# Kernel tuning notes

Measured on AMD Instinct MI355X. Metric: run time of the kernel, lower is better.

## Reference

```python
import jax, jax.numpy as jnp
import numpy as np

N = 100000
E = 1600000
F_IN = 128
DIM = 32
C = 2
BN_EPS = 1e-5


def setup_inputs() -> dict:
    key = jax.random.key(0)
    ks = jax.random.split(key, 24)
    s = 0.1
    inp = {
        'x': jax.random.normal(ks[0], (N, F_IN), dtype=jnp.float32),
        'edge_index': jax.random.randint(ks[1], (2, E), 0, N, dtype=jnp.int64),
        'edge_attr': jax.random.normal(ks[2], (E, 1), dtype=jnp.float32),
        'batch': jnp.zeros((N,), dtype=jnp.int64),
        # GIN layer 1 MLP: Linear(F_IN, DIM) -> ReLU -> Linear(DIM, DIM)
        'w1a': jax.random.normal(ks[3], (F_IN, DIM), dtype=jnp.float32) * s,
        'b1a': jnp.zeros((DIM,), dtype=jnp.float32),
        'w1b': jax.random.normal(ks[4], (DIM, DIM), dtype=jnp.float32) * s,
        'b1b': jnp.zeros((DIM,), dtype=jnp.float32),
        'g1': jnp.ones((DIM,), dtype=jnp.float32),
        'be1': jnp.zeros((DIM,), dtype=jnp.float32),
        # GIN layer 2
        'w2a': jax.random.normal(ks[5], (DIM, DIM), dtype=jnp.float32) * s,
        'b2a': jnp.zeros((DIM,), dtype=jnp.float32),
        'w2b': jax.random.normal(ks[6], (DIM, DIM), dtype=jnp.float32) * s,
        'b2b': jnp.zeros((DIM,), dtype=jnp.float32),
        'g2': jnp.ones((DIM,), dtype=jnp.float32),
        'be2': jnp.zeros((DIM,), dtype=jnp.float32),
        # GIN layer 3
        'w3a': jax.random.normal(ks[7], (DIM, DIM), dtype=jnp.float32) * s,
        'b3a': jnp.zeros((DIM,), dtype=jnp.float32),
        'w3b': jax.random.normal(ks[8], (DIM, DIM), dtype=jnp.float32) * s,
        'b3b': jnp.zeros((DIM,), dtype=jnp.float32),
        'g3': jnp.ones((DIM,), dtype=jnp.float32),
        'be3': jnp.zeros((DIM,), dtype=jnp.float32),
        # head
        'fw1': jax.random.normal(ks[9], (DIM, DIM), dtype=jnp.float32) * s,
        'fb1': jnp.zeros((DIM,), dtype=jnp.float32),
        'fw2': jax.random.normal(ks[10], (DIM, C), dtype=jnp.float32) * s,
        'fb2': jnp.zeros((C,), dtype=jnp.float32),
    }
    return inp


def _gin(x, src, dst, wa, ba, wb, bb):
    # GINConv with eps=0: h_i = MLP((1+eps)*x_i + sum_{j->i} x_j)
    agg = jax.ops.segment_sum(x[src], dst, num_segments=N)
    h = x + agg
    h = jax.nn.relu(h @ wa + ba) @ wb + bb
    return h


def _bn(h, g, b):
    # BatchNorm1d with batch statistics (training-mode normalization)
    mu = h.mean(axis=0)
    var = h.var(axis=0)  # biased, matches torch normalization
    return (h - mu) * jax.lax.rsqrt(var + BN_EPS) * g + b


def reference(x, edge_index, edge_attr, batch,
              w1a, b1a, w1b, b1b, g1, be1,
              w2a, b2a, w2b, b2b, g2, be2,
              w3a, b3a, w3b, b3b, g3, be3,
              fw1, fb1, fw2, fb2):
    src, dst = edge_index[0], edge_index[1]
    h = _bn(jax.nn.relu(_gin(x, src, dst, w1a, b1a, w1b, b1b)), g1, be1)
    h = _bn(jax.nn.relu(_gin(h, src, dst, w2a, b2a, w2b, b2b)), g2, be2)
    h = _bn(jax.nn.relu(_gin(h, src, dst, w3a, b3a, w3b, b3b)), g3, be3)
    h = jax.nn.relu(h @ fw1 + fb1)
    # dropout treated as identity (eval mode / deterministic reference)
    return h @ fw2 + fb2
```

## Files before the change

kernel.cpp:

```cpp
#include <hip/hip_runtime.h>

#define NNODES 100000
#define NEDGES 1600000
#define FIN 128
#define DIM 32
#define BN_EPS 1e-5f
#define NBUK ((NNODES + 255) >> 8)
#define CH 8192

__device__ __forceinline__ unsigned int f2bf2(float a, float b) {
    union { float f; unsigned int u; } ua, ub;
    ua.f = a; ub.f = b;
    const unsigned int ra = (ua.u + 0x7FFFu + ((ua.u >> 16) & 1u)) >> 16;
    const unsigned int rb = (ub.u + 0x7FFFu + ((ub.u >> 16) & 1u)) >> 16;
    return ra | (rb << 16);
}
__device__ __forceinline__ float bf_lo(unsigned int u) {
    union { unsigned int u; float f; } c; c.u = u << 16; return c.f;
}
__device__ __forceinline__ float bf_hi(unsigned int u) {
    union { unsigned int u; float f; } c; c.u = u & 0xFFFF0000u; return c.f;
}

__global__ void __launch_bounds__(256) k_proj1(const float* __restrict__ x,
                                               const float* __restrict__ w,
                                               unsigned int* __restrict__ zb) {
    const int i = blockIdx.x * 256 + threadIdx.x;
    if (i >= NNODES) return;
    const float4* xp = reinterpret_cast<const float4*>(x + (size_t)i * FIN);
    float acc[DIM];
#pragma unroll
    for (int c = 0; c < DIM; ++c) acc[c] = 0.f;

    for (int k0 = 0; k0 < FIN; k0 += 32) {
        float4 r[8];
#pragma unroll
        for (int q = 0; q < 8; ++q) r[q] = xp[k0 / 4 + q];
        float a[32];
#pragma unroll
        for (int q = 0; q < 8; ++q) {
            a[q * 4 + 0] = r[q].x; a[q * 4 + 1] = r[q].y;
            a[q * 4 + 2] = r[q].z; a[q * 4 + 3] = r[q].w;
        }
#pragma unroll
        for (int kk = 0; kk < 32; ++kk) {
            const float tk = a[kk];
#pragma unroll
            for (int c = 0; c < DIM; ++c)
                acc[c] += tk * w[(k0 + kk) * DIM + c];
        }
    }
    uint4* zp = reinterpret_cast<uint4*>(zb + (size_t)i * 16);
#pragma unroll
    for (int q = 0; q < 4; ++q)
        zp[q] = make_uint4(f2bf2(acc[q * 8 + 0], acc[q * 8 + 1]),
                           f2bf2(acc[q * 8 + 2], acc[q * 8 + 3]),
                           f2bf2(acc[q * 8 + 4], acc[q * 8 + 5]),
                           f2bf2(acc[q * 8 + 6], acc[q * 8 + 7]));
}

__global__ void k_bhist(const int* __restrict__ ei, int* __restrict__ bucketCnt) {
    __shared__ int cnt[NBUK];
    for (int i = threadIdx.x; i < NBUK; i += 256) cnt[i] = 0;
    __syncthreads();
    const int tid    = blockIdx.x * blockDim.x + threadIdx.x;
    const int stride = gridDim.x * blockDim.x;
    for (int e = tid; e < NEDGES; e += stride)
        atomicAdd(&cnt[ei[NEDGES + e] >> 8], 1);
    __syncthreads();
    for (int i = threadIdx.x; i < NBUK; i += 256)
        if (cnt[i]) atomicAdd(&bucketCnt[i], cnt[i]);
}

__global__ void k_bscan(const int* __restrict__ bucketCnt,
                        int* __restrict__ bbase, int* __restrict__ gcur,
                        float* __restrict__ stats) {
    __shared__ int sbuf[512];
    const int t = threadIdx.x;
    if (t < 192) stats[t] = 0.f;
    const int v = (t < NBUK) ? bucketCnt[t] : 0;
    sbuf[t] = v;
    __syncthreads();
    for (int off = 1; off < 512; off <<= 1) {
        const int u = (t >= off) ? sbuf[t - off] : 0;
        __syncthreads();
        sbuf[t] += u;
        __syncthreads();
    }
    if (t < NBUK) { const int ex = sbuf[t] - v; bbase[t] = ex; gcur[t] = ex; }
    if (t == 0) bbase[NBUK] = NEDGES;
}

__global__ void __launch_bounds__(256) k_bscatter(const int* __restrict__ ei,
                                                  int* __restrict__ gcur,
                                                  int* __restrict__ bucketed) {
    __shared__ int cnt[NBUK];
    __shared__ int base[NBUK];
    const int start = blockIdx.x * CH;
    const int end   = min(start + CH, NEDGES);
    for (int i = threadIdx.x; i < NBUK; i += 256) cnt[i] = 0;
    __syncthreads();
    for (int e = start + threadIdx.x; e < end; e += 256)
        atomicAdd(&cnt[ei[NEDGES + e] >> 8], 1);
    __syncthreads();
    for (int i = threadIdx.x; i < NBUK; i += 256) {
        const int c = cnt[i];
        base[i] = c ? atomicAdd(&gcur[i], c) : 0;
        cnt[i] = 0;
    }
    __syncthreads();
    for (int e = start + threadIdx.x; e < end; e += 256) {
        const int s = ei[e];
        const int d = ei[NEDGES + e];
        const int b = d >> 8;
        const int p = atomicAdd(&cnt[b], 1);
        bucketed[base[b] + p] = s | ((d & 255) << 17);
    }
}

__global__ void __launch_bounds__(256) k_bfill(const int* __restrict__ bucketed,
                                               const int* __restrict__ bbase,
                                               int* __restrict__ rowstart,
                                               int* __restrict__ deg,
                                               int* __restrict__ sorted_src) {
    __shared__ int dcnt[256], dsc[256], cur[256];
    const int b  = blockIdx.x;
    const int lo = bbase[b];
    const int hi = bbase[b + 1];
    const int t  = threadIdx.x;
    dcnt[t] = 0;
    __syncthreads();
    for (int p = lo + t; p < hi; p += 256)
        atomicAdd(&dcnt[bucketed[p] >> 17], 1);
    __syncthreads();
    const int myc = dcnt[t];
    dsc[t] = myc;
    __syncthreads();
    for (int off = 1; off < 256; off <<= 1) {
        const int u = (t >= off) ? dsc[t - off] : 0;
        __syncthreads();
        dsc[t] += u;
        __syncthreads();
    }
    const int ex = dsc[t] - myc;
    const int node = (b << 8) + t;
    if (node < NNODES) { rowstart[node] = lo + ex; deg[node] = myc; }
    dcnt[t] = ex;
    cur[t] = 0;
    __syncthreads();
    for (int p = lo + t; p < hi; p += 256) {
        const int v = bucketed[p];
        const int dl = v >> 17;
        const int pos = atomicAdd(&cur[dl], 1);
        sorted_src[lo + dcnt[dl] + pos] = v & 0x1FFFF;
    }
}

__global__ void k_gather_t(const unsigned int* __restrict__ zb,
                           const int* __restrict__ rowstart,
                           const int* __restrict__ deg,
                           const int* __restrict__ sorted_src,
                           const float* __restrict__ ba,
                           float* __restrict__ tbuf) {
    const int lane = threadIdx.x & 31;
    const int g    = lane >> 2;
    const int q    = lane & 3;
    const float4 baA = reinterpret_cast<const float4*>(ba)[q * 2];
    const float4 baB = reinterpret_cast<const float4*>(ba)[q * 2 + 1];
    const uint4* z4 = reinterpret_cast<const uint4*>(zb);
    const int hw  = (blockIdx.x * blockDim.x + threadIdx.x) >> 5;
    const int nhw = (gridDim.x * blockDim.x) >> 5;

    for (int i = hw; i < NNODES; i += nhw) {
        const int base = rowstart[i];
        const int cnt  = deg[i];
        float4 aA = make_float4(0.f, 0.f, 0.f, 0.f);
        float4 aB = make_float4(0.f, 0.f, 0.f, 0.f);
        float4 bA = make_float4(0.f, 0.f, 0.f, 0.f);
        float4 bB = make_float4(0.f, 0.f, 0.f, 0.f);
        for (int k0 = 0; k0 < cnt; k0 += 32) {
            int e = 0;
            if (k0 + lane < cnt) e = sorted_src[base + k0 + lane];
            const int m = min(32, cnt - k0);
            for (int j = 0; j < m; j += 16) {
                const int s0 = __shfl(e, j + g, 32);
                const int s1 = __shfl(e, j + 8 + g, 32);
                if (j + g < m) {
                    const uint4 v = z4[s0 * 4 + q];
                    aA.x += bf_lo(v.x); aA.y += bf_hi(v.x);
                    aA.z += bf_lo(v.y); aA.w += bf_hi(v.y);
                    aB.x += bf_lo(v.z); aB.y += bf_hi(v.z);
                    aB.z += bf_lo(v.w); aB.w += bf_hi(v.w);
                }
                if (j + 8 + g < m) {
                    const uint4 v = z4[s1 * 4 + q];
                    bA.x += bf_lo(v.x); bA.y += bf_hi(v.x);
                    bA.z += bf_lo(v.y); bA.w += bf_hi(v.y);
                    bB.x += bf_lo(v.z); bB.y += bf_hi(v.z);
                    bB.z += bf_lo(v.w); bB.w += bf_hi(v.w);
                }
            }
        }
        aA.x += bA.x; aA.y += bA.y; aA.z += bA.z; aA.w += bA.w;
        aB.x += bB.x; aB.y += bB.y; aB.z += bB.z; aB.w += bB.w;
#pragma unroll
        for (int mask = 4; mask <= 16; mask <<= 1) {
            aA.x += __shfl_xor(aA.x, mask, 32);
            aA.y += __shfl_xor(aA.y, mask, 32);
            aA.z += __shfl_xor(aA.z, mask, 32);
            aA.w += __shfl_xor(aA.w, mask, 32);
            aB.x += __shfl_xor(aB.x, mask, 32);
            aB.y += __shfl_xor(aB.y, mask, 32);
            aB.z += __shfl_xor(aB.z, mask, 32);
            aB.w += __shfl_xor(aB.w, mask, 32);
        }
        if (g == 0) {
            const uint4 v = z4[i * 4 + q];
            float4 tA, tB;
            tA.x = fmaxf(bf_lo(v.x) + aA.x + baA.x, 0.f);
            tA.y = fmaxf(bf_hi(v.x) + aA.y + baA.y, 0.f);
            tA.z = fmaxf(bf_lo(v.y) + aA.z + baA.z, 0.f);
            tA.w = fmaxf(bf_hi(v.y) + aA.w + baA.w, 0.f);
            tB.x = fmaxf(bf_lo(v.z) + aB.x + baB.x, 0.f);
            tB.y = fmaxf(bf_hi(v.z) + aB.y + baB.y, 0.f);
            tB.z = fmaxf(bf_lo(v.w) + aB.z + baB.z, 0.f);
            tB.w = fmaxf(bf_hi(v.w) + aB.w + baB.w, 0.f);
            float4* tp = reinterpret_cast<float4*>(tbuf + (size_t)i * DIM);
            tp[q * 2 + 0] = tA;
            tp[q * 2 + 1] = tB;
        }
    }
}

__global__ void __launch_bounds__(256) k_mlp2(float* __restrict__ hbuf,
                                              const float* __restrict__ wb,
                                              const float* __restrict__ bb,
                                              float* __restrict__ stats) {
    __shared__ float ssum[DIM], ssq[DIM];
    if (threadIdx.x < DIM) { ssum[threadIdx.x] = 0.f; ssq[threadIdx.x] = 0.f; }
    __syncthreads();

    const int i = blockIdx.x * 256 + threadIdx.x;
    const bool valid = i < NNODES;

    float a[DIM];
    if (valid) {
        const float4* tp = reinterpret_cast<const float4*>(hbuf + (size_t)i * DIM);
        float4 r[8];
#pragma unroll
        for (int qq = 0; qq < 8; ++qq) r[qq] = tp[qq];
#pragma unroll
        for (int qq = 0; qq < 8; ++qq) {
            a[qq * 4 + 0] = r[qq].x; a[qq * 4 + 1] = r[qq].y;
            a[qq * 4 + 2] = r[qq].z; a[qq * 4 + 3] = r[qq].w;
        }
    } else {
#pragma unroll
        for (int k = 0; k < DIM; ++k) a[k] = 0.f;
    }

    float acc[DIM];
#pragma unroll
    for (int c = 0; c < DIM; ++c) acc[c] = bb[c];
#pragma unroll
    for (int k = 0; k < DIM; ++k) {
        const float tk = a[k];
#pragma unroll
        for (int c = 0; c < DIM; ++c)
            acc[c] += tk * wb[k * DIM + c];
    }
#pragma unroll
    for (int c = 0; c < DIM; ++c) acc[c] = valid ? fmaxf(acc[c], 0.f) : 0.f;

    if (valid) {
        float4* hp = reinterpret_cast<float4*>(hbuf + (size_t)i * DIM);
#pragma unroll
        for (int qq = 0; qq < 8; ++qq)
            hp[qq] = make_float4(acc[qq * 4], acc[qq * 4 + 1], acc[qq * 4 + 2], acc[qq * 4 + 3]);
    }

    const int lane = threadIdx.x & 63;
    float lsum = 0.f, lsq = 0.f;
#pragma unroll
    for (int c = 0; c < DIM; ++c) {
        float v  = acc[c];
        float w2 = acc[c] * acc[c];
#pragma unroll
        for (int off = 1; off < 64; off <<= 1) {
            v  += __shfl_xor(v, off);
            w2 += __shfl_xor(w2, off);
        }
        if (lane == c) { lsum = v; lsq = w2; }
    }
    if (lane < DIM) {
        atomicAdd(&ssum[lane], lsum);
        atomicAdd(&ssq[lane], lsq);
    }
    __syncthreads();
    if (threadIdx.x < DIM) {
        atomicAdd(&stats[threadIdx.x],       ssum[threadIdx.x]);
        atomicAdd(&stats[DIM + threadIdx.x], ssq[threadIdx.x]);
    }
}

__global__ void __launch_bounds__(256) k_projbn(const float* __restrict__ h,
                                                const float* __restrict__ stats,
                                                const float* __restrict__ g,
                                                const float* __restrict__ be,
                                                const float* __restrict__ wa,
                                                unsigned int* __restrict__ zb) {
    const int t  = threadIdx.x;
    const int i  = blockIdx.x * 128 + (t & 127);
    const int ch = (t >> 7) * 16;
    if (i >= NNODES) return;
    const float4* hp = reinterpret_cast<const float4*>(h + (size_t)i * DIM);
    float4 r[8];
#pragma unroll
    for (int q = 0; q < 8; ++q) r[q] = hp[q];
    float a[DIM];
#pragma unroll
    for (int q = 0; q < 8; ++q) {
        a[q * 4 + 0] = r[q].x; a[q * 4 + 1] = r[q].y;
        a[q * 4 + 2] = r[q].z; a[q * 4 + 3] = r[q].w;
    }
    float acc[16];
#pragma unroll
    for (int c = 0; c < 16; ++c) acc[c] = 0.f;
#pragma unroll
    for (int k = 0; k < DIM; ++k) {
        const float mu  = stats[k] * (1.f / NNODES);
        const float var = stats[DIM + k] * (1.f / NNODES) - mu * mu;
        const float ss  = g[k] * rsqrtf(var + BN_EPS);
        const float st  = be[k] - mu * ss;
        const float tk  = a[k] * ss + st;
        const float* wr = wa + k * DIM + ch;
#pragma unroll
        for (int c = 0; c < 16; ++c)
            acc[c] += tk * wr[c];
    }
    uint4* zp = reinterpret_cast<uint4*>(zb + (size_t)i * 16 + ch / 2);
    zp[0] = make_uint4(f2bf2(acc[0], acc[1]),  f2bf2(acc[2], acc[3]),
                       f2bf2(acc[4], acc[5]),  f2bf2(acc[6], acc[7]));
    zp[1] = make_uint4(f2bf2(acc[8], acc[9]),  f2bf2(acc[10], acc[11]),
                       f2bf2(acc[12], acc[13]), f2bf2(acc[14], acc[15]));
}

__global__ void __launch_bounds__(256) k_head(const float* __restrict__ h,
                                              const float* __restrict__ stats,
                                              const float* __restrict__ g,
                                              const float* __restrict__ be,
                                              const float* __restrict__ fw1,
                                              const float* __restrict__ fb1,
                                              const float* __restrict__ fw2,
                                              const float* __restrict__ fb2,
                                              float* __restrict__ out) {
    const int i = blockIdx.x * 256 + threadIdx.x;
    if (i >= NNODES) return;
    const float4* hp = reinterpret_cast<const float4*>(h + (size_t)i * DIM);
    float4 r[8];
#pragma unroll
    for (int q = 0; q < 8; ++q) r[q] = hp[q];
    float a[DIM];
#pragma unroll
    for (int q = 0; q < 8; ++q) {
        a[q * 4 + 0] = r[q].x; a[q * 4 + 1] = r[q].y;
        a[q * 4 + 2] = r[q].z; a[q * 4 + 3] = r[q].w;
    }
    float acc[DIM];
#pragma unroll
    for (int c = 0; c < DIM; ++c) acc[c] = fb1[c];
#pragma unroll
    for (int k = 0; k < DIM; ++k) {
        const float mu  = stats[k] * (1.f / NNODES);
        const float var = stats[DIM + k] * (1.f / NNODES) - mu * mu;
        const float ss  = g[k] * rsqrtf(var + BN_EPS);
        const float st  = be[k] - mu * ss;
        const float tk  = a[k] * ss + st;
#pragma unroll
        for (int c = 0; c < DIM; ++c)
            acc[c] += tk * fw1[k * DIM + c];
    }
    float o0 = fb2[0], o1 = fb2[1];
#pragma unroll
    for (int c = 0; c < DIM; ++c) {
        const float u = fmaxf(acc[c], 0.f);
        o0 += u * fw2[c * 2 + 0];
        o1 += u * fw2[c * 2 + 1];
    }
    *reinterpret_cast<float2*>(&out[i * 2]) = make_float2(o0, o1);
}

extern "C" void kernel_launch(void* const* d_in, const int* in_sizes, int n_in,
                              void* d_out, int out_size, void* d_ws, size_t ws_size,
                              hipStream_t stream) {
    const float* x   = (const float*)d_in[0];
    const int*   ei  = (const int*)d_in[1];
    const float* w1a = (const float*)d_in[4];
    const float* b1a = (const float*)d_in[5];
    const float* w1b = (const float*)d_in[6];
    const float* b1b = (const float*)d_in[7];
    const float* g1  = (const float*)d_in[8];
    const float* be1 = (const float*)d_in[9];
    const float* w2a = (const float*)d_in[10];
    const float* b2a = (const float*)d_in[11];
    const float* w2b = (const float*)d_in[12];
    const float* b2b = (const float*)d_in[13];
    const float* g2  = (const float*)d_in[14];
    const float* be2 = (const float*)d_in[15];
    const float* w3a = (const float*)d_in[16];
    const float* b3a = (const float*)d_in[17];
    const float* w3b = (const float*)d_in[18];
    const float* b3b = (const float*)d_in[19];
    const float* g3  = (const float*)d_in[20];
    const float* be3 = (const float*)d_in[21];
    const float* fw1 = (const float*)d_in[22];
    const float* fb1 = (const float*)d_in[23];
    const float* fw2 = (const float*)d_in[24];
    const float* fb2 = (const float*)d_in[25];
    float* out = (float*)d_out;

    float* ws = (float*)d_ws;
    const size_t nf = (size_t)NNODES * DIM;
    unsigned int* zb = (unsigned int*)ws;
    float* h     = ws + nf;
    int*   bucketed = (int*)h;
    float* stats = ws + 2 * nf;
    int* rowstart   = (int*)(ws + 2 * nf + 192);
    int* deg        = rowstart + NNODES;
    int* sorted_src = deg + NNODES;
    int* bucketCnt  = sorted_src + NEDGES;
    int* bbase      = bucketCnt + NBUK;
    int* gcur       = bbase + NBUK + 1;

    const int TB = 256, NB_G = 2048;
    const int NB_TPN = (NNODES + 255) / 256;
    const int NB_PB  = (NNODES + 127) / 128;

    hipMemsetAsync(bucketCnt, 0, NBUK * sizeof(int), stream);

    k_bhist<<<512, TB, 0, stream>>>(ei, bucketCnt);
    k_bscan<<<1, 512, 0, stream>>>(bucketCnt, bbase, gcur, stats);
    k_bscatter<<<(NEDGES + CH - 1) / CH, TB, 0, stream>>>(ei, gcur, bucketed);
    k_bfill<<<NBUK, TB, 0, stream>>>(bucketed, bbase, rowstart, deg, sorted_src);

    k_proj1<<<NB_TPN, TB, 0, stream>>>(x, w1a, zb);
    k_gather_t<<<NB_G, TB, 0, stream>>>(zb, rowstart, deg, sorted_src, b1a, h);
    k_mlp2<<<NB_TPN, TB, 0, stream>>>(h, w1b, b1b, stats + 0);
    k_projbn<<<NB_PB, TB, 0, stream>>>(h, stats + 0, g1, be1, w2a, zb);
    k_gather_t<<<NB_G, TB, 0, stream>>>(zb, rowstart, deg, sorted_src, b2a, h);
    k_mlp2<<<NB_TPN, TB, 0, stream>>>(h, w2b, b2b, stats + 64);
    k_projbn<<<NB_PB, TB, 0, stream>>>(h, stats + 64, g2, be2, w3a, zb);
    k_gather_t<<<NB_G, TB, 0, stream>>>(zb, rowstart, deg, sorted_src, b3a, h);
    k_mlp2<<<NB_TPN, TB, 0, stream>>>(h, w3b, b3b, stats + 128);
    k_head<<<NB_TPN, TB, 0, stream>>>(h, stats + 128, g3, be3,
                                      fw1, fb1, fw2, fb2, out);
}
```

Before: 329.6 us.

## Split proj1 K-dimension across 4 lanes and simplify gather index loading

k_proj1 now assigns four lanes per node, each covering a quarter of the 128-wide input, with float4 weight loads and a shuffle reduction at the end. This gives four times the threads and makes the x reads from neighbouring lanes contiguous instead of strided per node. The gather kernel drops the 32-wide index preload plus shuffle broadcast and has each lane load its source index directly in 16-edge steps. This removes shuffle and branching overhead but issues more small redundant index loads.

Result: slower. 491.3 us (+49.1%).

```diff
diff --git a/kernel.cpp b/kernel.cpp
--- a/kernel.cpp
+++ b/kernel.cpp
@@ -25,38 +25,55 @@
 __global__ void __launch_bounds__(256) k_proj1(const float* __restrict__ x,
                                                const float* __restrict__ w,
                                                unsigned int* __restrict__ zb) {
-    const int i = blockIdx.x * 256 + threadIdx.x;
-    if (i >= NNODES) return;
-    const float4* xp = reinterpret_cast<const float4*>(x + (size_t)i * FIN);
+    const int t    = threadIdx.x;
+    const int l    = t & 63;
+    const int node = blockIdx.x * 64 + (t >> 6) * 16 + (l >> 2);
+    const int kq   = l & 3;
+    const bool valid = node < NNODES;
+
     float acc[DIM];
 #pragma unroll
     for (int c = 0; c < DIM; ++c) acc[c] = 0.f;
 
-    for (int k0 = 0; k0 < FIN; k0 += 32) {
+    if (valid) {
+        const float4* xp = reinterpret_cast<const float4*>(x + (size_t)node * FIN + kq * 32);
         float4 r[8];
 #pragma unroll
-        for (int q = 0; q < 8; ++q) r[q] = xp[k0 / 4 + q];
+        for (int q = 0; q < 8; ++q) r[q] = xp[q];
         float a[32];
 #pragma unroll
         for (int q = 0; q < 8; ++q) {
             a[q * 4 + 0] = r[q].x; a[q * 4 + 1] = r[q].y;
             a[q * 4 + 2] = r[q].z; a[q * 4 + 3] = r[q].w;
         }
+        const float4* w4 = reinterpret_cast<const float4*>(w) + (size_t)kq * 32 * 8;
 #pragma unroll
         for (int kk = 0; kk < 32; ++kk) {
             const float tk = a[kk];
 #pragma unroll
-            for (int c = 0; c < DIM; ++c)
-                acc[c] += tk * w[(k0 + kk) * DIM + c];
-        }
-    }
-    uint4* zp = reinterpret_cast<uint4*>(zb + (size_t)i * 16);
-#pragma unroll
-    for (int q = 0; q < 4; ++q)
-        zp[q] = make_uint4(f2bf2(acc[q * 8 + 0], acc[q * 8 + 1]),
-                           f2bf2(acc[q * 8 + 2], acc[q * 8 + 3]),
-                           f2bf2(acc[q * 8 + 4], acc[q * 8 + 5]),
-                           f2bf2(acc[q * 8 + 6], acc[q * 8 + 7]));
+            for (int cq = 0; cq < 8; ++cq) {
+                const float4 wv = w4[kk * 8 + cq];
+                acc[cq * 4 + 0] += tk * wv.x;
+                acc[cq * 4 + 1] += tk * wv.y;
+                acc[cq * 4 + 2] += tk * wv.z;
+                acc[cq * 4 + 3] += tk * wv.w;
+            }
+        }
+    }
+#pragma unroll
+    for (int c = 0; c < DIM; ++c) {
+        acc[c] += __shfl_xor(acc[c], 1);
+        acc[c] += __shfl_xor(acc[c], 2);
+    }
+    if (valid && kq == 0) {
+        uint4* zp = reinterpret_cast<uint4*>(zb + (size_t)node * 16);
+#pragma unroll
+        for (int q = 0; q < 4; ++q)
+            zp[q] = make_uint4(f2bf2(acc[q * 8 + 0], acc[q * 8 + 1]),
+                               f2bf2(acc[q * 8 + 2], acc[q * 8 + 3]),
+                               f2bf2(acc[q * 8 + 4], acc[q * 8 + 5]),
+                               f2bf2(acc[q * 8 + 6], acc[q * 8 + 7]));
+    }
 }
 
 __global__ void k_bhist(const int* __restrict__ ei, int* __restrict__ bucketCnt) {
@@ -178,27 +195,24 @@
         float4 aB = make_float4(0.f, 0.f, 0.f, 0.f);
         float4 bA = make_float4(0.f, 0.f, 0.f, 0.f);
         float4 bB = make_float4(0.f, 0.f, 0.f, 0.f);
-        for (int k0 = 0; k0 < cnt; k0 += 32) {
-            int e = 0;
-            if (k0 + lane < cnt) e = sorted_src[base + k0 + lane];
-            const int m = min(32, cnt - k0);
-            for (int j = 0; j < m; j += 16) {
-                const int s0 = __shfl(e, j + g, 32);
-                const int s1 = __shfl(e, j + 8 + g, 32);
-                if (j + g < m) {
-                    const uint4 v = z4[s0 * 4 + q];
-                    aA.x += bf_lo(v.x); aA.y += bf_hi(v.x);
-                    aA.z += bf_lo(v.y); aA.w += bf_hi(v.y);
-                    aB.x += bf_lo(v.z); aB.y += bf_hi(v.z);
-                    aB.z += bf_lo(v.w); aB.w += bf_hi(v.w);
-                }
-                if (j + 8 + g < m) {
-                    const uint4 v = z4[s1 * 4 + q];
-                    bA.x += bf_lo(v.x); bA.y += bf_hi(v.x);
-                    bA.z += bf_lo(v.y); bA.w += bf_hi(v.y);
-                    bB.x += bf_lo(v.z); bB.y += bf_hi(v.z);
-                    bB.z += bf_lo(v.w); bB.w += bf_hi(v.w);
-                }
+        for (int k0 = 0; k0 < cnt; k0 += 16) {
+            const int m = cnt - k0;
+            int s0 = -1, s1 = -1;
+            if (g < m)     s0 = sorted_src[base + k0 + g];
+            if (g + 8 < m) s1 = sorted_src[base + k0 + 8 + g];
+            if (s0 >= 0) {
+                const uint4 v = z4[s0 * 4 + q];
+                aA.x += bf_lo(v.x); aA.y += bf_hi(v.x);
+                aA.z += bf_lo(v.y); aA.w += bf_hi(v.y);
+                aB.x += bf_lo(v.z); aB.y += bf_hi(v.z);
+                aB.z += bf_lo(v.w); aB.w += bf_hi(v.w);
+            }
+            if (s1 >= 0) {
+                const uint4 v = z4[s1 * 4 + q];
+                bA.x += bf_lo(v.x); bA.y += bf_hi(v.x);
+                bA.z += bf_lo(v.y); bA.w += bf_hi(v.y);
+                bB.x += bf_lo(v.z); bB.y += bf_hi(v.z);
+                bB.z += bf_lo(v.w); bB.w += bf_hi(v.w);
             }
         }
         aA.x += bA.x; aA.y += bA.y; aA.z += bA.z; aA.w += bA.w;
@@ -434,6 +448,7 @@
 
     const int TB = 256, NB_G = 2048;
     const int NB_TPN = (NNODES + 255) / 256;
+    const int NB_P1  = (NNODES + 63) / 64;
     const int NB_PB  = (NNODES + 127) / 128;
 
     hipMemsetAsync(bucketCnt, 0, NBUK * sizeof(int), stream);
@@ -443,7 +458,7 @@
     k_bscatter<<<(NEDGES + CH - 1) / CH, TB, 0, stream>>>(ei, gcur, bucketed);
     k_bfill<<<NBUK, TB, 0, stream>>>(bucketed, bbase, rowstart, deg, sorted_src);
 
-    k_proj1<<<NB_TPN, TB, 0, stream>>>(x, w1a, zb);
+    k_proj1<<<NB_P1, TB, 0, stream>>>(x, w1a, zb);
     k_gather_t<<<NB_G, TB, 0, stream>>>(zb, rowstart, deg, sorted_src, b1a, h);
     k_mlp2<<<NB_TPN, TB, 0, stream>>>(h, w1b, b1b, stats + 0);
     k_projbn<<<NB_PB, TB, 0, stream>>>(h, stats + 0, g1, be1, w2a, zb);
```

## Fuse first projection with edge histogram and simplify gather index loading

Applied to the files above, without the earlier changes.

Merges the layer-1 input projection and the destination-bucket histogram into one launch, with different block ranges doing each job, so the two independent workloads share the GPU and one launch disappears. The gather loop now loads its source indices directly per 8-lane group in steps of 16 edges instead of loading 32 per lane and broadcasting with shuffles. This removes the shuffle traffic but issues more, smaller index loads. The fused kernel's block-index branching could also unbalance scheduling.

New measurement: 333.8 us. About the same (+1.3%).

```diff
diff --git a/kernel.cpp b/kernel.cpp
--- a/kernel.cpp
+++ b/kernel.cpp
@@ -7,6 +7,8 @@
 #define BN_EPS 1e-5f
 #define NBUK ((NNODES + 255) >> 8)
 #define CH 8192
+#define NB_P1 ((NNODES + 255) / 256)
+#define NB_H  512
 
 __device__ __forceinline__ unsigned int f2bf2(float a, float b) {
     union { float f; unsigned int u; } ua, ub;
@@ -22,9 +24,24 @@
     union { unsigned int u; float f; } c; c.u = u & 0xFFFF0000u; return c.f;
 }
 
-__global__ void __launch_bounds__(256) k_proj1(const float* __restrict__ x,
-                                               const float* __restrict__ w,
-                                               unsigned int* __restrict__ zb) {
+__global__ void __launch_bounds__(256) k_proj1_hist(const float* __restrict__ x,
+                                                    const float* __restrict__ w,
+                                                    unsigned int* __restrict__ zb,
+                                                    const int* __restrict__ ei,
+                                                    int* __restrict__ bucketCnt) {
+    __shared__ int cnt[NBUK];
+    if (blockIdx.x >= NB_P1) {
+        for (int i = threadIdx.x; i < NBUK; i += 256) cnt[i] = 0;
+        __syncthreads();
+        const int tid    = (blockIdx.x - NB_P1) * 256 + threadIdx.x;
+        const int stride = NB_H * 256;
+        for (int e = tid; e < NEDGES; e += stride)
+            atomicAdd(&cnt[ei[NEDGES + e] >> 8], 1);
+        __syncthreads();
+        for (int i = threadIdx.x; i < NBUK; i += 256)
+            if (cnt[i]) atomicAdd(&bucketCnt[i], cnt[i]);
+        return;
+    }
     const int i = blockIdx.x * 256 + threadIdx.x;
     if (i >= NNODES) return;
     const float4* xp = reinterpret_cast<const float4*>(x + (size_t)i * FIN);
@@ -57,19 +74,6 @@
                            f2bf2(acc[q * 8 + 2], acc[q * 8 + 3]),
                            f2bf2(acc[q * 8 + 4], acc[q * 8 + 5]),
                            f2bf2(acc[q * 8 + 6], acc[q * 8 + 7]));
-}
-
-__global__ void k_bhist(const int* __restrict__ ei, int* __restrict__ bucketCnt) {
-    __shared__ int cnt[NBUK];
-    for (int i = threadIdx.x; i < NBUK; i += 256) cnt[i] = 0;
-    __syncthreads();
-    const int tid    = blockIdx.x * blockDim.x + threadIdx.x;
-    const int stride = gridDim.x * blockDim.x;
-    for (int e = tid; e < NEDGES; e += stride)
-        atomicAdd(&cnt[ei[NEDGES + e] >> 8], 1);
-    __syncthreads();
-    for (int i = threadIdx.x; i < NBUK; i += 256)
-        if (cnt[i]) atomicAdd(&bucketCnt[i], cnt[i]);
 }
 
 __global__ void k_bscan(const int* __restrict__ bucketCnt,
@@ -178,27 +182,24 @@
         float4 aB = make_float4(0.f, 0.f, 0.f, 0.f);
         float4 bA = make_float4(0.f, 0.f, 0.f, 0.f);
         float4 bB = make_float4(0.f, 0.f, 0.f, 0.f);
-        for (int k0 = 0; k0 < cnt; k0 += 32) {
-            int e = 0;
-            if (k0 + lane < cnt) e = sorted_src[base + k0 + lane];
-            const int m = min(32, cnt - k0);
-            for (int j = 0; j < m; j += 16) {
-                const int s0 = __shfl(e, j + g, 32);
-                const int s1 = __shfl(e, j + 8 + g, 32);
-                if (j + g < m) {
-                    const uint4 v = z4[s0 * 4 + q];
-                    aA.x += bf_lo(v.x); aA.y += bf_hi(v.x);
-                    aA.z += bf_lo(v.y); aA.w += bf_hi(v.y);
-                    aB.x += bf_lo(v.z); aB.y += bf_hi(v.z);
-                    aB.z += bf_lo(v.w); aB.w += bf_hi(v.w);
-                }
-                if (j + 8 + g < m) {
-                    const uint4 v = z4[s1 * 4 + q];
-                    bA.x += bf_lo(v.x); bA.y += bf_hi(v.x);
-                    bA.z += bf_lo(v.y); bA.w += bf_hi(v.y);
-                    bB.x += bf_lo(v.z); bB.y += bf_hi(v.z);
-                    bB.z += bf_lo(v.w); bB.w += bf_hi(v.w);
-                }
+        for (int k0 = 0; k0 < cnt; k0 += 16) {
+            const int m = cnt - k0;
+            int s0 = -1, s1 = -1;
+            if (g < m)     s0 = sorted_src[base + k0 + g];
+            if (g + 8 < m) s1 = sorted_src[base + k0 + 8 + g];
+            if (s0 >= 0) {
+                const uint4 v = z4[s0 * 4 + q];
+                aA.x += bf_lo(v.x); aA.y += bf_hi(v.x);
+                aA.z += bf_lo(v.y); aA.w += bf_hi(v.y);
+                aB.x += bf_lo(v.z); aB.y += bf_hi(v.z);
+                aB.z += bf_lo(v.w); aB.w += bf_hi(v.w);
+            }
+            if (s1 >= 0) {
+                const uint4 v = z4[s1 * 4 + q];
+                bA.x += bf_lo(v.x); bA.y += bf_hi(v.x);
+                bA.z += bf_lo(v.y); bA.w += bf_hi(v.y);
+                bB.x += bf_lo(v.z); bB.y += bf_hi(v.z);
+                bB.z += bf_lo(v.w); bB.w += bf_hi(v.w);
             }
         }
         aA.x += bA.x; aA.y += bA.y; aA.z += bA.z; aA.w += bA.w;
@@ -438,12 +439,11 @@
 
     hipMemsetAsync(bucketCnt, 0, NBUK * sizeof(int), stream);
 
-    k_bhist<<<512, TB, 0, stream>>>(ei, bucketCnt);
+    k_proj1_hist<<<NB_P1 + NB_H, TB, 0, stream>>>(x, w1a, zb, ei, bucketCnt);
     k_bscan<<<1, 512, 0, stream>>>(bucketCnt, bbase, gcur, stats);
     k_bscatter<<<(NEDGES + CH - 1) / CH, TB, 0, stream>>>(ei, gcur, bucketed);
     k_bfill<<<NBUK, TB, 0, stream>>>(bucketed, bbase, rowstart, deg, sorted_src);
 
-    k_proj1<<<NB_TPN, TB, 0, stream>>>(x, w1a, zb);
     k_gather_t<<<NB_G, TB, 0, stream>>>(zb, rowstart, deg, sorted_src, b1a, h);
     k_mlp2<<<NB_TPN, TB, 0, stream>>>(h, w1b, b1b, stats + 0);
     k_projbn<<<NB_PB, TB, 0, stream>>>(h, stats + 0, g1, be1, w2a, zb);
```

## Fuse neighbor gather with second MLP linear and BN statistics per layer

Applied to the files above, without the earlier changes.

Merges the gather kernel and the per-node MLP/statistics kernel into one kernel per GIN layer. Each half-wave stages the aggregated hidden vector in shared memory, then computes one output channel per lane and accumulates sum and sum-of-squares locally before shared and global atomics. This removes the intermediate buffer round-trip and one launch per layer. The edge-index loads also change from a coalesced 32-wide load plus shuffles to direct 16-edge strided loads. The trade-offs are extra per-node work in the gather loop and a reliance on implicit intra-wave ordering for the shared staging.

New measurement: 405.2 us. 22.9% more time.

```diff
diff --git a/kernel.cpp b/kernel.cpp
--- a/kernel.cpp
+++ b/kernel.cpp
@@ -156,20 +156,32 @@
     }
 }
 
-__global__ void k_gather_t(const unsigned int* __restrict__ zb,
-                           const int* __restrict__ rowstart,
-                           const int* __restrict__ deg,
-                           const int* __restrict__ sorted_src,
-                           const float* __restrict__ ba,
-                           float* __restrict__ tbuf) {
+__global__ void __launch_bounds__(256) k_layer(const unsigned int* __restrict__ zb,
+                                               const int* __restrict__ rowstart,
+                                               const int* __restrict__ deg,
+                                               const int* __restrict__ sorted_src,
+                                               const float* __restrict__ ba,
+                                               const float* __restrict__ wb,
+                                               const float* __restrict__ bb,
+                                               float* __restrict__ h,
+                                               float* __restrict__ stats) {
+    __shared__ float tls[8][DIM];
+    __shared__ float ssum[DIM], ssq[DIM];
+    if (threadIdx.x < DIM) { ssum[threadIdx.x] = 0.f; ssq[threadIdx.x] = 0.f; }
+    __syncthreads();
+
     const int lane = threadIdx.x & 31;
+    const int hwl  = threadIdx.x >> 5;
     const int g    = lane >> 2;
     const int q    = lane & 3;
     const float4 baA = reinterpret_cast<const float4*>(ba)[q * 2];
     const float4 baB = reinterpret_cast<const float4*>(ba)[q * 2 + 1];
+    const float bbl  = bb[lane];
     const uint4* z4 = reinterpret_cast<const uint4*>(zb);
     const int hw  = (blockIdx.x * blockDim.x + threadIdx.x) >> 5;
     const int nhw = (gridDim.x * blockDim.x) >> 5;
+
+    float lsum = 0.f, lsq = 0.f;
 
     for (int i = hw; i < NNODES; i += nhw) {
         const int base = rowstart[i];
@@ -178,27 +190,24 @@
         float4 aB = make_float4(0.f, 0.f, 0.f, 0.f);
         float4 bA = make_float4(0.f, 0.f, 0.f, 0.f);
         float4 bB = make_float4(0.f, 0.f, 0.f, 0.f);
-        for (int k0 = 0; k0 < cnt; k0 += 32) {
-            int e = 0;
-            if (k0 + lane < cnt) e = sorted_src[base + k0 + lane];
-            const int m = min(32, cnt - k0);
-            for (int j = 0; j < m; j += 16) {
-                const int s0 = __shfl(e, j + g, 32);
-                const int s1 = __shfl(e, j + 8 + g, 32);
-                if (j + g < m) {
-                    const uint4 v = z4[s0 * 4 + q];
-                    aA.x += bf_lo(v.x); aA.y += bf_hi(v.x);
-                    aA.z += bf_lo(v.y); aA.w += bf_hi(v.y);
-                    aB.x += bf_lo(v.z); aB.y += bf_hi(v.z);
-                    aB.z += bf_lo(v.w); aB.w += bf_hi(v.w);
-                }
-                if (j + 8 + g < m) {
-                    const uint4 v = z4[s1 * 4 + q];
-                    bA.x += bf_lo(v.x); bA.y += bf_hi(v.x);
-                    bA.z += bf_lo(v.y); bA.w += bf_hi(v.y);
-                    bB.x += bf_lo(v.z); bB.y += bf_hi(v.z);
-                    bB.z += bf_lo(v.w); bB.w += bf_hi(v.w);
-                }
+        for (int k0 = 0; k0 < cnt; k0 += 16) {
+            const int m = cnt - k0;
+            int s0 = -1, s1 = -1;
+            if (g < m)     s0 = sorted_src[base + k0 + g];
+            if (g + 8 < m) s1 = sorted_src[base + k0 + 8 + g];
+            if (s0 >= 0) {
+                const uint4 v = z4[s0 * 4 + q];
+                aA.x += bf_lo(v.x); aA.y += bf_hi(v.x);
+                aA.z += bf_lo(v.y); aA.w += bf_hi(v.y);
+                aB.x += bf_lo(v.z); aB.y += bf_hi(v.z);
+                aB.z += bf_lo(v.w); aB.w += bf_hi(v.w);
+            }
+            if (s1 >= 0) {
+                const uint4 v = z4[s1 * 4 + q];
+                bA.x += bf_lo(v.x); bA.y += bf_hi(v.x);
+                bA.z += bf_lo(v.y); bA.w += bf_hi(v.y);
+                bB.x += bf_lo(v.z); bB.y += bf_hi(v.z);
+                bB.z += bf_lo(v.w); bB.w += bf_hi(v.w);
             }
         }
         aA.x += bA.x; aA.y += bA.y; aA.z += bA.z; aA.w += bA.w;
@@ -225,77 +234,25 @@
             tB.y = fmaxf(bf_hi(v.z) + aB.y + baB.y, 0.f);
             tB.z = fmaxf(bf_lo(v.w) + aB.z + baB.z, 0.f);
             tB.w = fmaxf(bf_hi(v.w) + aB.w + baB.w, 0.f);
-            float4* tp = reinterpret_cast<float4*>(tbuf + (size_t)i * DIM);
-            tp[q * 2 + 0] = tA;
-            tp[q * 2 + 1] = tB;
-        }
-    }
-}
-
-__global__ void __launch_bounds__(256) k_mlp2(float* __restrict__ hbuf,
-                                              const float* __restrict__ wb,
-                                              const float* __restrict__ bb,
-                                              float* __restrict__ stats) {
-    __shared__ float ssum[DIM], ssq[DIM];
-    if (threadIdx.x < DIM) { ssum[threadIdx.x] = 0.f; ssq[threadIdx.x] = 0.f; }
-    __syncthreads();
-
-    const int i = blockIdx.x * 256 + threadIdx.x;
-    const bool valid = i < NNODES;
-
-    float a[DIM];
-    if (valid) {
-        const float4* tp = reinterpret_cast<const float4*>(hbuf + (size_t)i * DIM);
-        float4 r[8];
-#pragma unroll
-        for (int qq = 0; qq < 8; ++qq) r[qq] = tp[qq];
-#pragma unroll
-        for (int qq = 0; qq < 8; ++qq) {
-            a[qq * 4 + 0] = r[qq].x; a[qq * 4 + 1] = r[qq].y;
-            a[qq * 4 + 2] = r[qq].z; a[qq * 4 + 3] = r[qq].w;
-        }
-    } else {
-#pragma unroll
-        for (int k = 0; k < DIM; ++k) a[k] = 0.f;
-    }
-
-    float acc[DIM];
-#pragma unroll
-    for (int c = 0; c < DIM; ++c) acc[c] = bb[c];
-#pragma unroll
-    for (int k = 0; k < DIM; ++k) {
-        const float tk = a[k];
-#pragma unroll
-        for (int c = 0; c < DIM; ++c)
-            acc[c] += tk * wb[k * DIM + c];
-    }
-#pragma unroll
-    for (int c = 0; c < DIM; ++c) acc[c] = valid ? fmaxf(acc[c], 0.f) : 0.f;
-
-    if (valid) {
-        float4* hp = reinterpret_cast<float4*>(hbuf + (size_t)i * DIM);
-#pragma unroll
-        for (int qq = 0; qq < 8; ++qq)
-            hp[qq] = make_float4(acc[qq * 4], acc[qq * 4 + 1], acc[qq * 4 + 2], acc[qq * 4 + 3]);
-    }
-
-    const int lane = threadIdx.x & 63;
-    float lsum = 0.f, lsq = 0.f;
-#pragma unroll
-    for (int c = 0; c < DIM; ++c) {
-        float v  = acc[c];
-        float w2 = acc[c] * acc[c];
-#pragma unroll
-        for (int off = 1; off < 64; off <<= 1) {
-            v  += __shfl_xor(v, off);
-            w2 += __shfl_xor(w2, off);
-        }
-        if (lane == c) { lsum = v; lsq = w2; }
-    }
-    if (lane < DIM) {
-        atomicAdd(&ssum[lane], lsum);
-        atomicAdd(&ssq[lane], lsq);
-    }
+            *reinterpret_cast<float4*>(&tls[hwl][q * 8 + 0]) = tA;
+            *reinterpret_cast<float4*>(&tls[hwl][q * 8 + 4]) = tB;
+        }
+        float acc = bbl;
+#pragma unroll
+        for (int k4 = 0; k4 < 8; ++k4) {
+            const float4 tv = *reinterpret_cast<const float4*>(&tls[hwl][k4 * 4]);
+            acc += tv.x * wb[(k4 * 4 + 0) * DIM + lane];
+            acc += tv.y * wb[(k4 * 4 + 1) * DIM + lane];
+            acc += tv.z * wb[(k4 * 4 + 2) * DIM + lane];
+            acc += tv.w * wb[(k4 * 4 + 3) * DIM + lane];
+        }
+        acc = fmaxf(acc, 0.f);
+        h[(size_t)i * DIM + lane] = acc;
+        lsum += acc;
+        lsq  += acc * acc;
+    }
+    atomicAdd(&ssum[lane], lsum);
+    atomicAdd(&ssq[lane], lsq);
     __syncthreads();
     if (threadIdx.x < DIM) {
         atomicAdd(&stats[threadIdx.x],       ssum[threadIdx.x]);
@@ -444,14 +401,14 @@
     k_bfill<<<NBUK, TB, 0, stream>>>(bucketed, bbase, rowstart, deg, sorted_src);
 
     k_proj1<<<NB_TPN, TB, 0, stream>>>(x, w1a, zb);
-    k_gather_t<<<NB_G, TB, 0, stream>>>(zb, rowstart, deg, sorted_src, b1a, h);
-    k_mlp2<<<NB_TPN, TB, 0, stream>>>(h, w1b, b1b, stats + 0);
+    k_layer<<<NB_G, TB, 0, stream>>>(zb, rowstart, deg, sorted_src,
+                                     b1a, w1b, b1b, h, stats + 0);
     k_projbn<<<NB_PB, TB, 0, stream>>>(h, stats + 0, g1, be1, w2a, zb);
-    k_gather_t<<<NB_G, TB, 0, stream>>>(zb, rowstart, deg, sorted_src, b2a, h);
-    k_mlp2<<<NB_TPN, TB, 0, stream>>>(h, w2b, b2b, stats + 64);
+    k_layer<<<NB_G, TB, 0, stream>>>(zb, rowstart, deg, sorted_src,
+                                     b2a, w2b, b2b, h, stats + 64);
     k_projbn<<<NB_PB, TB, 0, stream>>>(h, stats + 64, g2, be2, w3a, zb);
-    k_gather_t<<<NB_G, TB, 0, stream>>>(zb, rowstart, deg, sorted_src, b3a, h);
-    k_mlp2<<<NB_TPN, TB, 0, stream>>>(h, w3b, b3b, stats + 128);
+    k_layer<<<NB_G, TB, 0, stream>>>(zb, rowstart, deg, sorted_src,
+                                     b3a, w3b, b3b, h, stats + 128);
     k_head<<<NB_TPN, TB, 0, stream>>>(h, stats + 128, g3, be3,
                                       fw1, fb1, fw2, fb2, out);
 }
```
